# Kernel optimization log

Measured on AMD Instinct MI355X. Metric: run time of the kernel, lower is better.

## Reference

```python
import jax, jax.numpy as jnp
import numpy as np

D = 1024
H = 16
HD = D // H
B = 2
T = 2048


def setup_inputs() -> dict:
    key = jax.random.key(0)
    ks = jax.random.split(key, 5)
    x = jax.random.normal(ks[0], (B, T, D), dtype=jnp.float32)
    # PyTorch SDPA bool-mask semantics: True = attend. Causal lower-triangular.
    attn_mask = jnp.tril(jnp.ones((T, T), dtype=bool))
    w_qkv = jax.random.normal(ks[1], (3 * D, D), dtype=jnp.float32) * (1.0 / np.sqrt(D))
    b_qkv = jax.random.normal(ks[2], (3 * D,), dtype=jnp.float32) * 0.02
    w_proj = jax.random.normal(ks[3], (D, D), dtype=jnp.float32) * (1.0 / np.sqrt(D))
    b_proj = jax.random.normal(ks[4], (D,), dtype=jnp.float32) * 0.02
    return {"x": x, "attn_mask": attn_mask, "w_qkv": w_qkv, "b_qkv": b_qkv,
            "w_proj": w_proj, "b_proj": b_proj}


def reference(x, attn_mask, w_qkv, b_qkv, w_proj, b_proj):
    b, t, d = x.shape
    # fused QKV projection (torch Linear: y = x @ W.T + b)
    qkv = jnp.einsum('btd,ed->bte', x, w_qkv) + b_qkv  # [B,T,3D]
    q, k, v = jnp.split(qkv, 3, axis=-1)
    # [B,T,D] -> [B,H,T,hd]
    def heads(z):
        return z.reshape(b, t, H, HD).transpose(0, 2, 1, 3)
    q, k, v = heads(q), heads(k), heads(v)
    scale = 1.0 / jnp.sqrt(jnp.asarray(HD, dtype=x.dtype))
    scores = jnp.einsum('bhqd,bhkd->bhqk', q, k) * scale  # [B,H,T,T]
    neg_inf = jnp.asarray(jnp.finfo(x.dtype).min, dtype=x.dtype)
    scores = jnp.where(attn_mask, scores, neg_inf)
    attn = jax.nn.softmax(scores, axis=-1)
    y = jnp.einsum('bhqk,bhkd->bhqd', attn, v)  # [B,H,T,hd]
    y = y.transpose(0, 2, 1, 3).reshape(b, t, d)
    y = jnp.einsum('btd,ed->bte', y, w_proj) + b_proj
    return y
```

## Files before the change

kernel.cpp:

```cpp
#include <hip/hip_runtime.h>
#include <hip/hip_bf16.h>
#include <math.h>

#define D_MODEL 1024
#define NHEAD   16
#define HDIM    64
#define BATCH   2
#define SEQ     2048
#define MTOT    (BATCH * SEQ)

typedef unsigned short u16;
typedef unsigned int u32;
typedef short short8 __attribute__((ext_vector_type(8)));
typedef float floatx4 __attribute__((ext_vector_type(4)));

#define LOG2E 1.44269504088896340736f

static __device__ __forceinline__ u16 f2b(float f) {
  union { __hip_bfloat16 h; u16 u; } cv;
  cv.h = __float2bfloat16(f);
  return cv.u;
}

typedef const __attribute__((address_space(1))) unsigned int guint;
typedef __attribute__((address_space(3))) unsigned int luint;
static __device__ __forceinline__ void gl_lds16(const u16* g, u16* l) {
  __builtin_amdgcn_global_load_lds((guint*)g, (luint*)l, 16, 0, 0);
}

__global__ __launch_bounds__(256) void cast3_f2b(
    const float* __restrict__ a, u16* __restrict__ ao, int na,
    const float* __restrict__ b, u16* __restrict__ bo, int nb,
    const float* __restrict__ c, u16* __restrict__ co) {
  int i = (blockIdx.x * 256 + threadIdx.x) * 4;
  const float* src;
  u16* dst;
  if (i < na) {
    src = a + i;
    dst = ao + i;
  } else if (i < na + nb) {
    src = b + (i - na);
    dst = bo + (i - na);
  } else {
    src = c + (i - na - nb);
    dst = co + (i - na - nb);
  }
  float4 v = *(const float4*)src;
  ushort4 o;
  o.x = f2b(v.x);
  o.y = f2b(v.y);
  o.z = f2b(v.z);
  o.w = f2b(v.w);
  *(ushort4*)dst = o;
}

template <int MODE, int AR>
__global__ __launch_bounds__(256) void gemm_bt_bf16(
    const u16* __restrict__ A, const u16* __restrict__ Bm,
    const float* __restrict__ bias, u16* __restrict__ Cq, u16* __restrict__ Ck,
    u16* __restrict__ Cvt, float* __restrict__ Cf, int M, int N, int K) {
  constexpr int MI = AR / 32;
  constexpr int SMREQ = 2 * (AR + 128) * 32;
  constexpr int SM = (MODE == 0) ? (SMREQ > 17408 ? SMREQ : 17408) : SMREQ;
  __shared__ u16 smem[SM];
  u16(*As)[AR][32] = (u16(*)[AR][32])smem;
  u16(*Bs)[128][32] = (u16(*)[128][32])(smem + 2 * AR * 32);

  const int tid = threadIdx.x;
  const int lane = tid & 63;
  const int wave = tid >> 6;
  const int wm = (wave >> 1) * (AR / 2);
  const int wn = (wave & 1) * 64;
  const int quad = lane >> 4;
  const int l15 = lane & 15;
  const int m0 = blockIdx.y * AR;
  const int n0 = blockIdx.x * 128;

  const int srow = wave * 16 + (lane >> 2);
  const int k8 = (lane & 3) * 8;

  const u16* gA0 = A + (size_t)(m0 + srow) * K + k8;
  const u16* gA1 = A + (size_t)(m0 + srow + 64) * K + k8;
  const u16* gB0 = Bm + (size_t)(n0 + srow) * K + k8;
  const u16* gB1 = Bm + (size_t)(n0 + srow + 64) * K + k8;

  floatx4 acc[MI][4];
#pragma unroll
  for (int i = 0; i < MI; ++i)
#pragma unroll
    for (int j = 0; j < 4; ++j)
#pragma unroll
      for (int e = 0; e < 4; ++e) acc[i][j][e] = 0.0f;

  gl_lds16(gA0, &As[0][srow][k8]);
  if (AR == 128) gl_lds16(gA1, &As[0][srow + 64][k8]);
  gl_lds16(gB0, &Bs[0][srow][k8]);
  gl_lds16(gB1, &Bs[0][srow + 64][k8]);

  const int niter = K / 32;
  for (int kt = 0; kt < niter; ++kt) {
    const int cur = kt & 1;
    __syncthreads();
    if (kt + 1 < niter) {
      const int k0n = (kt + 1) * 32;
      gl_lds16(gA0 + k0n, &As[cur ^ 1][srow][k8]);
      if (AR == 128) gl_lds16(gA1 + k0n, &As[cur ^ 1][srow + 64][k8]);
      gl_lds16(gB0 + k0n, &Bs[cur ^ 1][srow][k8]);
      gl_lds16(gB1 + k0n, &Bs[cur ^ 1][srow + 64][k8]);
    }
    short8 af[MI], bf[4];
#pragma unroll
    for (int i = 0; i < MI; ++i)
      af[i] = *(const short8*)&As[cur][wm + i * 16 + l15][quad * 8];
#pragma unroll
    for (int j = 0; j < 4; ++j)
      bf[j] = *(const short8*)&Bs[cur][wn + j * 16 + l15][quad * 8];
#pragma unroll
    for (int i = 0; i < MI; ++i)
#pragma unroll
      for (int j = 0; j < 4; ++j)
        acc[i][j] = __builtin_amdgcn_mfma_f32_16x16x32_bf16(af[i], bf[j],
                                                            acc[i][j], 0, 0, 0);
  }

  if (MODE == 0) {
    const int nbase = n0 + wn;
    const int sel = nbase >> 10;
    const int h = (nbase >> 6) & (NHEAD - 1);
    if (sel == 2) {
#pragma unroll
      for (int j = 0; j < 4; ++j) {
        const int n = nbase + j * 16 + l15;
        const float bv = bias[n];
        const int d = n & (HDIM - 1);
#pragma unroll
        for (int i = 0; i < MI; ++i) {
          const int mb = m0 + wm + i * 16 + quad * 4;
          const int b = mb >> 11;
          const int t = mb & (SEQ - 1);
          ushort4 o4;
          o4.x = f2b(acc[i][j][0] + bv);
          o4.y = f2b(acc[i][j][1] + bv);
          o4.z = f2b(acc[i][j][2] + bv);
          o4.w = f2b(acc[i][j][3] + bv);
          *(ushort4*)(Cvt + ((size_t)(b * NHEAD + h) * HDIM + d) * SEQ + t) = o4;
        }
      }
    } else {
      u16* dst = (sel == 0) ? Cq : Ck;
      __syncthreads();
      u16(*Ct)[68] = (u16(*)[68])(smem + wave * 4352);
#pragma unroll
      for (int j = 0; j < 4; ++j) {
        const float bv = bias[nbase + j * 16 + l15];
#pragma unroll
        for (int i = 0; i < MI; ++i)
#pragma unroll
          for (int r = 0; r < 4; ++r)
            Ct[i * 16 + quad * 4 + r][j * 16 + l15] = f2b(acc[i][j][r] + bv);
      }
      const int mb0 = m0 + wm;
      const int b = mb0 >> 11;
      const int t0 = mb0 & (SEQ - 1);
      u16* rowbase = dst + ((size_t)(b * NHEAD + h) * SEQ + t0) * HDIM;
      const int tr = lane >> 3;
      const int d8 = (lane & 7) * 8;
#pragma unroll
      for (int p = 0; p < 8; ++p) {
        const int row = p * 8 + tr;
        *(short8*)(rowbase + (size_t)row * HDIM + d8) =
            *(const short8*)&Ct[row][d8];
      }
    }
  } else {
#pragma unroll
    for (int j = 0; j < 4; ++j) {
      const int n = n0 + wn + j * 16 + l15;
      const float bv = bias[n];
#pragma unroll
      for (int i = 0; i < MI; ++i) {
        const int mb = m0 + wm + i * 16 + quad * 4;
#pragma unroll
        for (int r = 0; r < 4; ++r)
          Cf[(size_t)(mb + r) * N + n] = acc[i][j][r] + bv;
      }
    }
  }
}

__global__ __launch_bounds__(256) void flash_mfma(const u16* __restrict__ Qg,
                                                  const u16* __restrict__ Kg,
                                                  const u16* __restrict__ Vtg,
                                                  u16* __restrict__ Yb) {
  __shared__ u16 Qs[64][76];
  __shared__ u16 Ks[64][76];
  __shared__ u16 Vt[80][76];
  __shared__ u16 Pb[64][76];

  const int tid = threadIdx.x;
  const int lane = tid & 63;
  const int wave = tid >> 6;
  const int wrow = wave * 16;
  const int quad = lane >> 4;
  const int l15 = lane & 15;
  const int bh = blockIdx.y;
  const int b = bh >> 4;
  const int h = bh & (NHEAD - 1);

  const u16* Qp = Qg + (size_t)bh * SEQ * HDIM;
  const u16* Kp = Kg + (size_t)bh * SEQ * HDIM;
  const u16* Vp = Vtg + (size_t)bh * HDIM * SEQ;

  const int srow = tid >> 2;
  const int sc = (tid & 3) * 16;

  const float scale2 = 0.125f * LOG2E;

  for (int idx = tid; idx < 16 * 38; idx += 256) {
    const int row = 64 + idx / 38;
    const int c2 = (idx % 38) * 2;
    *(u32*)&Vt[row][c2] = (row == 64 && c2 < 64) ? 0x3F803F80u : 0u;
  }

#pragma unroll
  for (int phase = 0; phase < 2; ++phase) {
    const int qt = phase == 0 ? (16 + blockIdx.x) : (15 - blockIdx.x);
    const int q0 = qt * 64;

    __syncthreads();
    {
      const u16* qsrc = Qp + (size_t)(q0 + srow) * HDIM + sc;
      short8 qv0 = *(const short8*)qsrc;
      short8 qv1 = *(const short8*)(qsrc + 8);
      *(short8*)&Qs[srow][sc] = qv0;
      *(short8*)&Qs[srow][sc + 8] = qv1;
    }

    floatx4 o[5];
#pragma unroll
    for (int c = 0; c < 5; ++c)
#pragma unroll
      for (int e = 0; e < 4; ++e) o[c][e] = 0.0f;

    const int nkt = qt + 1;
    short8 kv0 = *(const short8*)(Kp + (size_t)srow * HDIM + sc);
    short8 kv1 = *(const short8*)(Kp + (size_t)srow * HDIM + sc + 8);
    short8 vv0 = *(const short8*)(Vp + (size_t)srow * SEQ + sc);
    short8 vv1 = *(const short8*)(Vp + (size_t)srow * SEQ + sc + 8);

    for (int kt = 0; kt < nkt; ++kt) {
      const int k0 = kt * 64;
      __syncthreads();
      *(short8*)&Ks[srow][sc] = kv0;
      *(short8*)&Ks[srow][sc + 8] = kv1;
      *(short8*)&Vt[srow][sc] = vv0;
      *(short8*)&Vt[srow][sc + 8] = vv1;
      __syncthreads();
      if (kt + 1 < nkt) {
        const u16* kp = Kp + (size_t)(k0 + 64 + srow) * HDIM + sc;
        const u16* vp = Vp + (size_t)srow * SEQ + k0 + 64 + sc;
        kv0 = *(const short8*)kp;
        kv1 = *(const short8*)(kp + 8);
        vv0 = *(const short8*)vp;
        vv1 = *(const short8*)(vp + 8);
      }

      short8 aq[2], bk[4][2];
#pragma unroll
      for (int kk = 0; kk < 2; ++kk)
        aq[kk] = *(const short8*)&Qs[wrow + l15][kk * 32 + quad * 8];
#pragma unroll
      for (int c = 0; c < 4; ++c)
#pragma unroll
        for (int kk = 0; kk < 2; ++kk)
          bk[c][kk] = *(const short8*)&Ks[c * 16 + l15][kk * 32 + quad * 8];

      floatx4 s[4];
#pragma unroll
      for (int c = 0; c < 4; ++c) {
#pragma unroll
        for (int e = 0; e < 4; ++e) s[c][e] = 0.0f;
        s[c] = __builtin_amdgcn_mfma_f32_16x16x32_bf16(aq[0], bk[c][0], s[c],
                                                       0, 0, 0);
        s[c] = __builtin_amdgcn_mfma_f32_16x16x32_bf16(aq[1], bk[c][1], s[c],
                                                       0, 0, 0);
      }

      const bool msk = (kt == nkt - 1);
      const int prow = wrow + quad * 4;
#pragma unroll
      for (int c = 0; c < 4; ++c)
#pragma unroll
        for (int r = 0; r < 4; ++r) {
          float v = s[c][r] * scale2;
          if (msk) {
            const int row = q0 + prow + r;
            const int col = k0 + c * 16 + l15;
            if (col > row) v = -INFINITY;
          }
          Pb[prow + r][c * 16 + l15] = f2b(exp2f(v));
        }

      short8 ap[2];
#pragma unroll
      for (int kk = 0; kk < 2; ++kk)
        ap[kk] = *(const short8*)&Pb[wrow + l15][kk * 32 + quad * 8];
#pragma unroll
      for (int c = 0; c < 5; ++c) {
        short8 bv0 = *(const short8*)&Vt[c * 16 + l15][quad * 8];
        short8 bv1 = *(const short8*)&Vt[c * 16 + l15][32 + quad * 8];
        o[c] = __builtin_amdgcn_mfma_f32_16x16x32_bf16(ap[0], bv0, o[c], 0, 0,
                                                       0);
        o[c] = __builtin_amdgcn_mfma_f32_16x16x32_bf16(ap[1], bv1, o[c], 0, 0,
                                                       0);
      }
    }

#pragma unroll
    for (int r = 0; r < 4; ++r) {
      const float lr = __shfl(o[4][r], lane & 48);
      const float inv = 1.0f / lr;
      const int t = q0 + wrow + quad * 4 + r;
#pragma unroll
      for (int c = 0; c < 4; ++c)
        Yb[((size_t)b * SEQ + t) * D_MODEL + h * HDIM + c * 16 + l15] =
            f2b(o[c][r] * inv);
    }
  }
}

extern "C" void kernel_launch(void* const* d_in, const int* in_sizes, int n_in,
                              void* d_out, int out_size, void* d_ws,
                              size_t ws_size, hipStream_t stream) {
  const float* x = (const float*)d_in[0];
  const float* w_qkv = (const float*)d_in[2];
  const float* b_qkv = (const float*)d_in[3];
  const float* w_proj = (const float*)d_in[4];
  const float* b_proj = (const float*)d_in[5];
  float* out = (float*)d_out;

  const size_t nx = (size_t)MTOT * D_MODEL;
  const size_t nwq = (size_t)3 * D_MODEL * D_MODEL;
  const size_t nwp = (size_t)D_MODEL * D_MODEL;
  const size_t nqkv = (size_t)BATCH * NHEAD * SEQ * HDIM;

  u16* xb = (u16*)d_ws;
  u16* wqb = xb + nx;
  u16* wpb = wqb + nwq;
  u16* qb = wpb + nwp;
  u16* kb = qb + nqkv;
  u16* vtb = kb + nqkv;
  u16* yb = vtb + nqkv;

  cast3_f2b<<<dim3((nx + nwq + nwp) / 1024), dim3(256), 0, stream>>>(
      x, xb, (int)nx, w_qkv, wqb, (int)nwq, w_proj, wpb);

  gemm_bt_bf16<0, 128><<<dim3(24, 32), dim3(256), 0, stream>>>(
      xb, wqb, b_qkv, qb, kb, vtb, nullptr, MTOT, 3 * D_MODEL, D_MODEL);
  flash_mfma<<<dim3(16, BATCH * NHEAD), dim3(256), 0, stream>>>(qb, kb, vtb,
                                                                yb);
  gemm_bt_bf16<1, 64><<<dim3(8, 64), dim3(256), 0, stream>>>(
      yb, wpb, b_proj, nullptr, nullptr, nullptr, out, MTOT, D_MODEL, D_MODEL);
}
```

Baseline: 195.2 us.

## Double-buffer K/V LDS tiles, load Q into registers, use fast exp2

```diff
diff --git a/kernel.cpp b/kernel.cpp
--- a/kernel.cpp
+++ b/kernel.cpp
@@ -15,6 +15,12 @@
 typedef float floatx4 __attribute__((ext_vector_type(4)));
 
 #define LOG2E 1.44269504088896340736f
+
+#if __has_builtin(__builtin_amdgcn_exp2f)
+#define EXP2(x) __builtin_amdgcn_exp2f(x)
+#else
+#define EXP2(x) exp2f(x)
+#endif
 
 static __device__ __forceinline__ u16 f2b(float f) {
   union { __hip_bfloat16 h; u16 u; } cv;
@@ -192,9 +198,8 @@
                                                   const u16* __restrict__ Kg,
                                                   const u16* __restrict__ Vtg,
                                                   u16* __restrict__ Yb) {
-  __shared__ u16 Qs[64][76];
-  __shared__ u16 Ks[64][76];
-  __shared__ u16 Vt[80][76];
+  __shared__ u16 Ks[2][64][76];
+  __shared__ u16 Vt[2][80][76];
   __shared__ u16 Pb[64][76];
 
   const int tid = threadIdx.x;
@@ -216,11 +221,13 @@
 
   const float scale2 = 0.125f * LOG2E;
 
-  for (int idx = tid; idx < 16 * 38; idx += 256) {
-    const int row = 64 + idx / 38;
-    const int c2 = (idx % 38) * 2;
-    *(u32*)&Vt[row][c2] = (row == 64 && c2 < 64) ? 0x3F803F80u : 0u;
-  }
+#pragma unroll
+  for (int bufi = 0; bufi < 2; ++bufi)
+    for (int idx = tid; idx < 16 * 38; idx += 256) {
+      const int row = 64 + idx / 38;
+      const int c2 = (idx % 38) * 2;
+      *(u32*)&Vt[bufi][row][c2] = (row == 64 && c2 < 64) ? 0x3F803F80u : 0u;
+    }
 
 #pragma unroll
   for (int phase = 0; phase < 2; ++phase) {
@@ -228,12 +235,12 @@
     const int q0 = qt * 64;
 
     __syncthreads();
+
+    short8 aq[2];
     {
-      const u16* qsrc = Qp + (size_t)(q0 + srow) * HDIM + sc;
-      short8 qv0 = *(const short8*)qsrc;
-      short8 qv1 = *(const short8*)(qsrc + 8);
-      *(short8*)&Qs[srow][sc] = qv0;
-      *(short8*)&Qs[srow][sc + 8] = qv1;
+      const u16* qrow = Qp + (size_t)(q0 + wrow + l15) * HDIM + quad * 8;
+      aq[0] = *(const short8*)qrow;
+      aq[1] = *(const short8*)(qrow + 32);
     }
 
     floatx4 o[5];
@@ -250,11 +257,11 @@
 
     for (int kt = 0; kt < nkt; ++kt) {
       const int k0 = kt * 64;
-      __syncthreads();
-      *(short8*)&Ks[srow][sc] = kv0;
-      *(short8*)&Ks[srow][sc + 8] = kv1;
-      *(short8*)&Vt[srow][sc] = vv0;
-      *(short8*)&Vt[srow][sc + 8] = vv1;
+      const int buf = kt & 1;
+      *(short8*)&Ks[buf][srow][sc] = kv0;
+      *(short8*)&Ks[buf][srow][sc + 8] = kv1;
+      *(short8*)&Vt[buf][srow][sc] = vv0;
+      *(short8*)&Vt[buf][srow][sc + 8] = vv1;
       __syncthreads();
       if (kt + 1 < nkt) {
         const u16* kp = Kp + (size_t)(k0 + 64 + srow) * HDIM + sc;
@@ -265,15 +272,13 @@
         vv1 = *(const short8*)(vp + 8);
       }
 
-      short8 aq[2], bk[4][2];
-#pragma unroll
-      for (int kk = 0; kk < 2; ++kk)
-        aq[kk] = *(const short8*)&Qs[wrow + l15][kk * 32 + quad * 8];
+      short8 bk[4][2];
 #pragma unroll
       for (int c = 0; c < 4; ++c)
 #pragma unroll
         for (int kk = 0; kk < 2; ++kk)
-          bk[c][kk] = *(const short8*)&Ks[c * 16 + l15][kk * 32 + quad * 8];
+          bk[c][kk] =
+              *(const short8*)&Ks[buf][c * 16 + l15][kk * 32 + quad * 8];
 
       floatx4 s[4];
 #pragma unroll
@@ -298,7 +303,7 @@
             const int col = k0 + c * 16 + l15;
             if (col > row) v = -INFINITY;
           }
-          Pb[prow + r][c * 16 + l15] = f2b(exp2f(v));
+          Pb[prow + r][c * 16 + l15] = f2b(EXP2(v));
         }
 
       short8 ap[2];
@@ -307,8 +312,8 @@
         ap[kk] = *(const short8*)&Pb[wrow + l15][kk * 32 + quad * 8];
 #pragma unroll
       for (int c = 0; c < 5; ++c) {
-        short8 bv0 = *(const short8*)&Vt[c * 16 + l15][quad * 8];
-        short8 bv1 = *(const short8*)&Vt[c * 16 + l15][32 + quad * 8];
+        short8 bv0 = *(const short8*)&Vt[buf][c * 16 + l15][quad * 8];
+        short8 bv1 = *(const short8*)&Vt[buf][c * 16 + l15][32 + quad * 8];
         o[c] = __builtin_amdgcn_mfma_f32_16x16x32_bf16(ap[0], bv0, o[c], 0, 0,
                                                        0);
         o[c] = __builtin_amdgcn_mfma_f32_16x16x32_bf16(ap[1], bv1, o[c], 0, 0,
```

Result: faster. 188.2 us (-3.6%).
